# Kernel tuning notes

Measured on AMD Instinct MI355X. Metric: run time of the kernel, lower is better.

Reference implementation:

```python
import jax, jax.numpy as jnp
import numpy as np

N = 250000      # total nodes = B * NN
E = 4000000     # edges (avg degree 16)
NODE = 4        # node_size
EDGE = 1        # edge_size
HID = 32        # hidden_dim
NN = 50         # nnodes per graph
NF = 3          # num_factories


def setup_inputs() -> dict:
    key = jax.random.key(0)
    ks = jax.random.split(key, 10)
    def glorot(k, shp, fan_in):
        return (jax.random.normal(k, shp, jnp.float32) / np.sqrt(fan_in)).astype(jnp.float32)
    x = jax.random.normal(ks[0], (N, NODE), jnp.float32)
    edge_index = jax.random.randint(ks[1], (2, E), 0, N, dtype=jnp.int64)
    edge_attr = jax.random.normal(ks[2], (E, EDGE), jnp.float32)
    high = jnp.ones((NF,), jnp.float32)
    D_in = 2 * NODE + EDGE
    D_cat = NODE + HID
    W1 = glorot(ks[3], (D_in, HID), D_in); b1 = jnp.zeros((HID,), jnp.float32)
    W2 = glorot(ks[4], (HID, HID), HID);   b2 = jnp.zeros((HID,), jnp.float32)
    Wc = glorot(ks[5], (D_cat, 1), D_cat);  bc = jnp.zeros((1,), jnp.float32)
    Wmu = glorot(ks[6], (D_cat, 1), D_cat); bmu = jnp.zeros((1,), jnp.float32)
    Wsig = glorot(ks[7], (D_cat, 1), D_cat); bsig = jnp.zeros((1,), jnp.float32)
    return dict(x=x, edge_index=edge_index, edge_attr=edge_attr, high=high,
                W1=W1, b1=b1, W2=W2, b2=b2, Wc=Wc, bc=bc,
                Wmu=Wmu, bmu=bmu, Wsig=Wsig, bsig=bsig)


def reference(x, edge_index, edge_attr, high, W1, b1, W2, b2, Wc, bc, Wmu, bmu, Wsig, bsig):
    # EdgeConv (flow='target_to_source', aggr='add'): x_i = x[row], x_j = x[col], scatter-add at row
    row, col = edge_index[0], edge_index[1]
    msg_in = jnp.concatenate([x[row], x[col], edge_attr], axis=1)      # [E, 2*NODE+EDGE]
    msg = jax.nn.relu(msg_in @ W1 + b1) @ W2 + b2                      # [E, HID]
    agg = jax.ops.segment_sum(msg, row, num_segments=x.shape[0])       # [N, HID]
    x_pp = jnp.concatenate([x, agg], axis=1).reshape(-1, NN, NODE + HID)  # [B, NN, D_cat]
    tail = x_pp[:, -NF:]                                               # [B, NF, D_cat]
    alpha = jax.nn.softplus((tail @ Wmu + bmu).squeeze(-1) + 1e-20) + 1e-20   # [B, NF]
    beta = jax.nn.softplus((tail @ Wsig + bsig).squeeze(-1) + 1e-20) + 1e-20  # [B, NF]
    conc = jax.nn.softplus((x_pp @ Wc + bc).squeeze(-1) + 1e-10)       # [B, NN]
    inventory_act = conc / (conc.sum() + 1e-20)                        # deterministic Dirichlet mean-style
    order_act = alpha / (alpha + beta) * high                          # deterministic Beta mean * high
    return jnp.concatenate([inventory_act, order_act], axis=1)         # [B, NN+NF]
```

## Files before the change

kernel.cpp:

```cpp
#include <hip/hip_runtime.h>

#define N_NODES 250000
#define N_EDGES 4000000
#define HID 32
#define NN 50
#define NF 3
#define OUT_COLS (NN + NF)

#define NB 512
#define NBKT ((N_NODES + NB - 1) / NB)
#define PCHUNK 4096
#define NPBLK ((N_EDGES + PCHUNK - 1) / PCHUNK)
#define BCAP_SLOT 8832

typedef float float2v __attribute__((ext_vector_type(2)));

__device__ __forceinline__ float softplus_f(float v) {
    return fmaxf(v, 0.0f) + log1pf(expf(-fabsf(v)));
}

__device__ __forceinline__ float2v pk_fma(float a, float2v b, float2v c) {
    float2v av = {a, a};
    return __builtin_elementwise_fma(av, b, c);
}

__global__ __launch_bounds__(1024, 8) void part_kernel(
    const int* __restrict__ ei, const float* __restrict__ ea,
    int* __restrict__ gcursor, int2* __restrict__ bpay)
{
    __shared__ int2 srec[PCHUNK];
    __shared__ int  gdst[PCHUNK];
    __shared__ int hist[NBKT];
    __shared__ int excl[NBKT];
    __shared__ int gbase[NBKT];
    __shared__ int wsum[16];

    int t = threadIdx.x;
    int lane = t & 63, wid = t >> 6;
    int cbb = blockIdx.x * PCHUNK;
    int cnt = N_EDGES - cbb; if (cnt > PCHUNK) cnt = PCHUNK;

    for (int i = t; i < NBKT; i += 1024) hist[i] = 0;
    __syncthreads();

    int e0 = cbb + t * 4;
    int r[4], rk[4];
    bool full = (e0 + 4 <= N_EDGES);
    if (full) {
        int4 ra = *(const int4*)(ei + e0);
        r[0] = ra.x; r[1] = ra.y; r[2] = ra.z; r[3] = ra.w;
    } else {
        #pragma unroll
        for (int j = 0; j < 4; j++) r[j] = (e0 + j < N_EDGES) ? ei[e0 + j] : 0;
    }
    #pragma unroll
    for (int j = 0; j < 4; j++)
        rk[j] = (e0 + j < N_EDGES) ? atomicAdd(&hist[r[j] >> 9], 1) : 0;
    __syncthreads();

    int hv = (t < NBKT) ? hist[t] : 0;
    int v = hv;
    #pragma unroll
    for (int off = 1; off < 64; off <<= 1) {
        int u = __shfl_up(v, off, 64);
        if (lane >= off) v += u;
    }
    if (lane == 63) wsum[wid] = v;
    __syncthreads();
    if (wid == 0) {
        int w = (lane < 16) ? wsum[lane] : 0;
        #pragma unroll
        for (int off = 1; off < 16; off <<= 1) {
            int u = __shfl_up(w, off, 64);
            if (lane >= off) w += u;
        }
        if (lane < 16) wsum[lane] = w;
    }
    __syncthreads();
    int wbase = (wid > 0) ? wsum[wid - 1] : 0;
    int myExcl = wbase + (v - hv);
    if (t < NBKT) {
        excl[t] = myExcl;
        int base = 0;
        if (hv > 0) base = atomicAdd(&gcursor[t], hv);
        gbase[t] = t * BCAP_SLOT + base;
    }
    __syncthreads();

    if (full) {
        int4 ca = *(const int4*)(ei + N_EDGES + e0);
        float4 aa = *(const float4*)(ea + e0);
        int c[4] = {ca.x, ca.y, ca.z, ca.w};
        float a[4] = {aa.x, aa.y, aa.z, aa.w};
        #pragma unroll
        for (int j = 0; j < 4; j++) {
            int bb = r[j] >> 9;
            int lrow = r[j] & (NB - 1);
            int slot = excl[bb] + rk[j];
            int gpos = gbase[bb] + rk[j];
            srec[slot] = make_int2(c[j] | (lrow << 18), __float_as_int(a[j]));
            gdst[slot] = (gpos < (bb + 1) * BCAP_SLOT) ? gpos : -1;
        }
    } else {
        #pragma unroll
        for (int j = 0; j < 4; j++) {
            if (e0 + j < N_EDGES) {
                int bb = r[j] >> 9;
                int lrow = r[j] & (NB - 1);
                int col  = ei[N_EDGES + e0 + j];
                float at = ea[e0 + j];
                int slot = excl[bb] + rk[j];
                int gpos = gbase[bb] + rk[j];
                srec[slot] = make_int2(col | (lrow << 18), __float_as_int(at));
                gdst[slot] = (gpos < (bb + 1) * BCAP_SLOT) ? gpos : -1;
            }
        }
    }
    __syncthreads();

    for (int s = t; s < cnt; s += 1024) {
        int g = gdst[s];
        if (g >= 0) bpay[g] = srec[s];
    }
}

__global__ __launch_bounds__(512, 4) void bucket_kernel(
    const int2* __restrict__ bpay, const int* __restrict__ gcursor,
    const float* __restrict__ x,
    const float* __restrict__ W1, const float* __restrict__ b1,
    const float* __restrict__ W2, const float* __restrict__ b2,
    const float* __restrict__ Wc, const float* __restrict__ bc,
    const float* __restrict__ Wmu, const float* __restrict__ bmu,
    const float* __restrict__ Wsig, const float* __restrict__ bsig,
    const float* __restrict__ high,
    float* __restrict__ sum_out, float* __restrict__ out)
{
    __shared__ int2 srec[BCAP_SLOT];
    __shared__ int hist[NB];
    __shared__ int nbeg[NB];
    __shared__ int perm[NB];
    __shared__ int dhist[64];
    __shared__ int wsum[8];
    __shared__ float bsum[8];
    __shared__ float fW[3][32];
    __shared__ float fB[3];

    int b = blockIdx.x;
    int t = threadIdx.x;
    int lane = t & 63, wid = t >> 6;
    int beg = b * BCAP_SLOT;
    int cnt = gcursor[b]; if (cnt > BCAP_SLOT) cnt = BCAP_SLOT;

    hist[t] = 0;
    if (t < 96) {
        int vsel = t >> 5;
        int k = t & 31;
        const float* Wv = (vsel == 0) ? Wc : (vsel == 1) ? Wmu : Wsig;
        float f = 0.0f;
        #pragma unroll
        for (int j = 0; j < 32; j++) f = fmaf(W2[k * 32 + j], Wv[4 + j], f);
        fW[vsel][k] = f;
    } else if (t < 99) {
        int vsel = t - 96;
        const float* Wv = (vsel == 0) ? Wc : (vsel == 1) ? Wmu : Wsig;
        float f = 0.0f;
        #pragma unroll
        for (int j = 0; j < 32; j++) f = fmaf(b2[j], Wv[4 + j], f);
        fB[vsel] = f;
    }
    __syncthreads();

    int2 rec[18];
    int rk[18];
    #pragma unroll
    for (int k = 0; k < 9; k++) {
        int s = (k * 512 + t) * 2;
        int4 pp = *(const int4*)(bpay + beg + s);
        rec[2 * k]     = make_int2(pp.x, pp.y);
        rec[2 * k + 1] = make_int2(pp.z, pp.w);
        rk[2 * k]     = (s < cnt)     ? atomicAdd(&hist[(pp.x >> 18) & (NB - 1)], 1) : 0;
        rk[2 * k + 1] = (s + 1 < cnt) ? atomicAdd(&hist[(pp.z >> 18) & (NB - 1)], 1) : 0;
    }
    __syncthreads();

    int hv = hist[t];
    int v = hv;
    #pragma unroll
    for (int off = 1; off < 64; off <<= 1) {
        int u = __shfl_up(v, off, 64);
        if (lane >= off) v += u;
    }
    if (lane == 63) wsum[wid] = v;
    __syncthreads();
    if (wid == 0) {
        int w = (lane < 8) ? wsum[lane] : 0;
        #pragma unroll
        for (int off = 1; off < 8; off <<= 1) {
            int u = __shfl_up(w, off, 64);
            if (lane >= off) w += u;
        }
        if (lane < 8) wsum[lane] = w;
    }
    __syncthreads();
    int wbase = (wid > 0) ? wsum[wid - 1] : 0;
    nbeg[t] = wbase + (v - hv);
    __syncthreads();

    #pragma unroll
    for (int k = 0; k < 9; k++) {
        int s = (k * 512 + t) * 2;
        if (s < cnt) {
            int lrow = (rec[2 * k].x >> 18) & (NB - 1);
            srec[nbeg[lrow] + rk[2 * k]] = rec[2 * k];
        }
        if (s + 1 < cnt) {
            int lrow = (rec[2 * k + 1].x >> 18) & (NB - 1);
            srec[nbeg[lrow] + rk[2 * k + 1]] = rec[2 * k + 1];
        }
    }

    int bin = min(hv, 63);
    if (t < 64) dhist[t] = 0;
    __syncthreads();
    atomicAdd(&dhist[bin], 1);
    __syncthreads();
    if (wid == 0) {
        int dv = dhist[lane];
        int sv = dv;
        #pragma unroll
        for (int off = 1; off < 64; off <<= 1) {
            int u = __shfl_up(sv, off, 64);
            if (lane >= off) sv += u;
        }
        dhist[lane] = sv - dv;
    }
    __syncthreads();
    int pos = atomicAdd(&dhist[bin], 1);
    perm[pos] = t;
    __syncthreads();

    int tt = perm[t];
    int n = b * NB + tt;
    bool valid = (n < N_NODES);
    int nn = valid ? n : 0;
    int deg = valid ? hist[tt] : 0;
    int s0 = nbeg[tt];

    float4 xr = *(const float4*)(x + 4 * (size_t)nn);

    const float2v* W1v = (const float2v*)W1;
    const float2v* b1v = (const float2v*)b1;

    float2v arow[16];
    #pragma unroll
    for (int k2 = 0; k2 < 16; k2++) {
        float2v a = b1v[k2];
        a = pk_fma(xr.x, W1v[0 * 16 + k2], a);
        a = pk_fma(xr.y, W1v[1 * 16 + k2], a);
        a = pk_fma(xr.z, W1v[2 * 16 + k2], a);
        a = pk_fma(xr.w, W1v[3 * 16 + k2], a);
        arow[k2] = a;
    }

    float2v acc2[16];
    #pragma unroll
    for (int j2 = 0; j2 < 16; j2++) { float2v z = {0.f, 0.f}; acc2[j2] = z; }

    float mk0[4], ev0[4];
    float4 xc0[4];
    #pragma unroll
    for (int j = 0; j < 4; j++) {
        bool ok = j < deg;
        int idx = ok ? (s0 + j) : 0;
        int2 rr = srec[idx];
        mk0[j] = ok ? 1.0f : 0.0f;
        int col = ok ? (rr.x & 0x3FFFF) : 0;
        ev0[j] = ok ? __int_as_float(rr.y) : 0.0f;
        xc0[j] = *(const float4*)(x + 4 * (size_t)col);
    }

    for (int c = 0; c < deg; c += 4) {
        int c1 = c + 4;
        float mk1[4], ev1[4];
        float4 xc1[4];
        #pragma unroll
        for (int j = 0; j < 4; j++) {
            bool ok = (c1 + j) < deg;
            int idx = ok ? (s0 + c1 + j) : 0;
            int2 rr = srec[idx];
            mk1[j] = ok ? 1.0f : 0.0f;
            int col = ok ? (rr.x & 0x3FFFF) : 0;
            ev1[j] = ok ? __int_as_float(rr.y) : 0.0f;
            xc1[j] = *(const float4*)(x + 4 * (size_t)col);
        }

        #pragma unroll
        for (int k2 = 0; k2 < 16; k2++) {
            float2v w4 = W1v[4 * 16 + k2];
            float2v w5 = W1v[5 * 16 + k2];
            float2v w6 = W1v[6 * 16 + k2];
            float2v w7 = W1v[7 * 16 + k2];
            float2v w8 = W1v[8 * 16 + k2];
            #pragma unroll
            for (int j = 0; j < 4; j++) {
                float2v a = arow[k2];
                a = pk_fma(xc0[j].x, w4, a);
                a = pk_fma(xc0[j].y, w5, a);
                a = pk_fma(xc0[j].z, w6, a);
                a = pk_fma(xc0[j].w, w7, a);
                a = pk_fma(ev0[j],   w8, a);
                float2v zero = {0.0f, 0.0f};
                a = __builtin_elementwise_max(a, zero);
                float2v mm = {mk0[j], mk0[j]};
                acc2[k2] = __builtin_elementwise_fma(a, mm, acc2[k2]);
            }
        }

        #pragma unroll
        for (int j = 0; j < 4; j++) {
            mk0[j] = mk1[j]; ev0[j] = ev1[j]; xc0[j] = xc1[j];
        }
    }

    float c_val = 0.0f;
    if (valid) {
        float* accf = (float*)acc2;
        float fdeg = (float)deg;

        float zc = fmaf(fdeg, fB[0], bc[0]);
        zc = fmaf(xr.x, Wc[0], zc);
        zc = fmaf(xr.y, Wc[1], zc);
        zc = fmaf(xr.z, Wc[2], zc);
        zc = fmaf(xr.w, Wc[3], zc);
        #pragma unroll
        for (int j = 0; j < 32; j++) zc = fmaf(accf[j], fW[0][j], zc);
        c_val = softplus_f(zc + 1e-10f);

        int g = n / NN;
        int i = n - g * NN;
        out[(size_t)g * OUT_COLS + i] = c_val;

        if (i >= NN - NF) {
            float zm = fmaf(fdeg, fB[1], bmu[0]);
            float zs = fmaf(fdeg, fB[2], bsig[0]);
            zm = fmaf(xr.x, Wmu[0], zm);   zs = fmaf(xr.x, Wsig[0], zs);
            zm = fmaf(xr.y, Wmu[1], zm);   zs = fmaf(xr.y, Wsig[1], zs);
            zm = fmaf(xr.z, Wmu[2], zm);   zs = fmaf(xr.z, Wsig[2], zs);
            zm = fmaf(xr.w, Wmu[3], zm);   zs = fmaf(xr.w, Wsig[3], zs);
            #pragma unroll
            for (int j = 0; j < 32; j++) {
                zm = fmaf(accf[j], fW[1][j], zm);
                zs = fmaf(accf[j], fW[2][j], zs);
            }
            float alpha = softplus_f(zm + 1e-20f) + 1e-20f;
            float beta  = softplus_f(zs + 1e-20f) + 1e-20f;
            int k = i - (NN - NF);
            out[(size_t)g * OUT_COLS + NN + k] = alpha / (alpha + beta) * high[k];
        }
    }

    float s = c_val;
    #pragma unroll
    for (int off = 32; off > 0; off >>= 1) s += __shfl_down(s, off, 64);
    if (lane == 0) bsum[wid] = s;
    __syncthreads();
    if (t == 0) {
        float tt2 = 0.0f;
        #pragma unroll
        for (int j = 0; j < 8; j++) tt2 += bsum[j];
        atomicAdd(sum_out, tt2);
    }
}

__global__ __launch_bounds__(256) void div_kernel(
    const float* __restrict__ sum_in, float* __restrict__ out)
{
    int n = blockIdx.x * 256 + threadIdx.x;
    if (n >= N_NODES) return;
    float inv = 1.0f / (*sum_in + 1e-20f);
    int g = n / NN;
    int i = n - g * NN;
    out[(size_t)g * OUT_COLS + i] *= inv;
}

extern "C" void kernel_launch(void* const* d_in, const int* in_sizes, int n_in,
                              void* d_out, int out_size, void* d_ws, size_t ws_size,
                              hipStream_t stream)
{
    const float* x    = (const float*)d_in[0];
    const int*   ei   = (const int*)d_in[1];
    const float* ea   = (const float*)d_in[2];
    const float* high = (const float*)d_in[3];
    const float* W1   = (const float*)d_in[4];
    const float* b1   = (const float*)d_in[5];
    const float* W2   = (const float*)d_in[6];
    const float* b2   = (const float*)d_in[7];
    const float* Wc   = (const float*)d_in[8];
    const float* bc   = (const float*)d_in[9];
    const float* Wmu  = (const float*)d_in[10];
    const float* bmu  = (const float*)d_in[11];
    const float* Wsig = (const float*)d_in[12];
    const float* bsig = (const float*)d_in[13];
    float* out = (float*)d_out;

    char* ws = (char*)d_ws;
    int2*  bpay    = (int2*)ws;
    int*   gcursor = (int*)(ws + 34550784);
    float* ssum    = (float*)(ws + 34552832);

    hipMemsetAsync(gcursor, 0, 2052, stream);

    part_kernel<<<NPBLK, 1024, 0, stream>>>(ei, ea, gcursor, bpay);
    bucket_kernel<<<NBKT, 512, 0, stream>>>(
        bpay, gcursor, x, W1, b1, W2, b2, Wc, bc, Wmu, bmu, Wsig, bsig,
        high, ssum, out);
    div_kernel<<<(N_NODES + 255) / 256, 256, 0, stream>>>(ssum, out);
}
```

Baseline: 186.0 us.

## Halve node bucket size and split each node's edges across two threads

After: 201.2 us. +8.2%, slower.

```diff
diff --git a/kernel.cpp b/kernel.cpp
--- a/kernel.cpp
+++ b/kernel.cpp
@@ -7,11 +7,11 @@
 #define NF 3
 #define OUT_COLS (NN + NF)
 
-#define NB 512
+#define NB 256
 #define NBKT ((N_NODES + NB - 1) / NB)
 #define PCHUNK 4096
 #define NPBLK ((N_EDGES + PCHUNK - 1) / PCHUNK)
-#define BCAP_SLOT 8832
+#define BCAP_SLOT 4544
 
 typedef float float2v __attribute__((ext_vector_type(2)));
 
@@ -55,7 +55,7 @@
     }
     #pragma unroll
     for (int j = 0; j < 4; j++)
-        rk[j] = (e0 + j < N_EDGES) ? atomicAdd(&hist[r[j] >> 9], 1) : 0;
+        rk[j] = (e0 + j < N_EDGES) ? atomicAdd(&hist[r[j] >> 8], 1) : 0;
     __syncthreads();
 
     int hv = (t < NBKT) ? hist[t] : 0;
@@ -94,7 +94,7 @@
         float a[4] = {aa.x, aa.y, aa.z, aa.w};
         #pragma unroll
         for (int j = 0; j < 4; j++) {
-            int bb = r[j] >> 9;
+            int bb = r[j] >> 8;
             int lrow = r[j] & (NB - 1);
             int slot = excl[bb] + rk[j];
             int gpos = gbase[bb] + rk[j];
@@ -105,7 +105,7 @@
         #pragma unroll
         for (int j = 0; j < 4; j++) {
             if (e0 + j < N_EDGES) {
-                int bb = r[j] >> 9;
+                int bb = r[j] >> 8;
                 int lrow = r[j] & (NB - 1);
                 int col  = ei[N_EDGES + e0 + j];
                 float at = ea[e0 + j];
@@ -140,7 +140,7 @@
     __shared__ int nbeg[NB];
     __shared__ int perm[NB];
     __shared__ int dhist[64];
-    __shared__ int wsum[8];
+    __shared__ int wsum[4];
     __shared__ float bsum[8];
     __shared__ float fW[3][32];
     __shared__ float fB[3];
@@ -151,17 +151,17 @@
     int beg = b * BCAP_SLOT;
     int cnt = gcursor[b]; if (cnt > BCAP_SLOT) cnt = BCAP_SLOT;
 
-    hist[t] = 0;
-    if (t < 96) {
-        int vsel = t >> 5;
+    if (t < NB) hist[t] = 0;
+    if (t >= 256 && t < 352) {
+        int vsel = (t - 256) >> 5;
         int k = t & 31;
         const float* Wv = (vsel == 0) ? Wc : (vsel == 1) ? Wmu : Wsig;
         float f = 0.0f;
         #pragma unroll
         for (int j = 0; j < 32; j++) f = fmaf(W2[k * 32 + j], Wv[4 + j], f);
         fW[vsel][k] = f;
-    } else if (t < 99) {
-        int vsel = t - 96;
+    } else if (t >= 352 && t < 355) {
+        int vsel = t - 352;
         const float* Wv = (vsel == 0) ? Wc : (vsel == 1) ? Wmu : Wsig;
         float f = 0.0f;
         #pragma unroll
@@ -170,12 +170,13 @@
     }
     __syncthreads();
 
-    int2 rec[18];
-    int rk[18];
-    #pragma unroll
-    for (int k = 0; k < 9; k++) {
+    int2 rec[10];
+    int rk[10];
+    #pragma unroll
+    for (int k = 0; k < 5; k++) {
         int s = (k * 512 + t) * 2;
-        int4 pp = *(const int4*)(bpay + beg + s);
+        int sc = (s <= BCAP_SLOT - 2) ? s : 0;
+        int4 pp = *(const int4*)(bpay + beg + sc);
         rec[2 * k]     = make_int2(pp.x, pp.y);
         rec[2 * k + 1] = make_int2(pp.z, pp.w);
         rk[2 * k]     = (s < cnt)     ? atomicAdd(&hist[(pp.x >> 18) & (NB - 1)], 1) : 0;
@@ -183,31 +184,33 @@
     }
     __syncthreads();
 
-    int hv = hist[t];
+    int hv = (t < NB) ? hist[t] : 0;
     int v = hv;
     #pragma unroll
     for (int off = 1; off < 64; off <<= 1) {
         int u = __shfl_up(v, off, 64);
         if (lane >= off) v += u;
     }
-    if (lane == 63) wsum[wid] = v;
+    if (lane == 63 && wid < 4) wsum[wid] = v;
     __syncthreads();
     if (wid == 0) {
-        int w = (lane < 8) ? wsum[lane] : 0;
-        #pragma unroll
-        for (int off = 1; off < 8; off <<= 1) {
+        int w = (lane < 4) ? wsum[lane] : 0;
+        #pragma unroll
+        for (int off = 1; off < 4; off <<= 1) {
             int u = __shfl_up(w, off, 64);
             if (lane >= off) w += u;
         }
-        if (lane < 8) wsum[lane] = w;
-    }
-    __syncthreads();
-    int wbase = (wid > 0) ? wsum[wid - 1] : 0;
-    nbeg[t] = wbase + (v - hv);
-    __syncthreads();
-
-    #pragma unroll
-    for (int k = 0; k < 9; k++) {
+        if (lane < 4) wsum[lane] = w;
+    }
+    __syncthreads();
+    if (t < NB) {
+        int wbase = (wid > 0) ? wsum[wid - 1] : 0;
+        nbeg[t] = wbase + (v - hv);
+    }
+    __syncthreads();
+
+    #pragma unroll
+    for (int k = 0; k < 5; k++) {
         int s = (k * 512 + t) * 2;
         if (s < cnt) {
             int lrow = (rec[2 * k].x >> 18) & (NB - 1);
@@ -219,10 +222,10 @@
         }
     }
 
+    if (t < 64) dhist[t] = 0;
+    __syncthreads();
     int bin = min(hv, 63);
-    if (t < 64) dhist[t] = 0;
-    __syncthreads();
-    atomicAdd(&dhist[bin], 1);
+    if (t < NB) atomicAdd(&dhist[bin], 1);
     __syncthreads();
     if (wid == 0) {
         int dv = dhist[lane];
@@ -235,16 +238,22 @@
         dhist[lane] = sv - dv;
     }
     __syncthreads();
-    int pos = atomicAdd(&dhist[bin], 1);
-    perm[pos] = t;
-    __syncthreads();
-
-    int tt = perm[t];
-    int n = b * NB + tt;
+    if (t < NB) {
+        int pos = atomicAdd(&dhist[bin], 1);
+        perm[pos] = t;
+    }
+    __syncthreads();
+
+    int pr = t >> 1;
+    int slice = t & 1;
+    int node = perm[pr];
+    int n = b * NB + node;
     bool valid = (n < N_NODES);
     int nn = valid ? n : 0;
-    int deg = valid ? hist[tt] : 0;
-    int s0 = nbeg[tt];
+    int deg = valid ? hist[node] : 0;
+    int half = (deg + 1) >> 1;
+    int myCnt = slice ? (deg - half) : half;
+    int s0 = nbeg[node] + slice * half;
 
     float4 xr = *(const float4*)(x + 4 * (size_t)nn);
 
@@ -270,7 +279,7 @@
     float4 xc0[4];
     #pragma unroll
     for (int j = 0; j < 4; j++) {
-        bool ok = j < deg;
+        bool ok = j < myCnt;
         int idx = ok ? (s0 + j) : 0;
         int2 rr = srec[idx];
         mk0[j] = ok ? 1.0f : 0.0f;
@@ -279,13 +288,13 @@
         xc0[j] = *(const float4*)(x + 4 * (size_t)col);
     }
 
-    for (int c = 0; c < deg; c += 4) {
+    for (int c = 0; c < myCnt; c += 4) {
         int c1 = c + 4;
         float mk1[4], ev1[4];
         float4 xc1[4];
         #pragma unroll
         for (int j = 0; j < 4; j++) {
-            bool ok = (c1 + j) < deg;
+            bool ok = (c1 + j) < myCnt;
             int idx = ok ? (s0 + c1 + j) : 0;
             int2 rr = srec[idx];
             mk1[j] = ok ? 1.0f : 0.0f;
@@ -322,9 +331,12 @@
         }
     }
 
+    float* accf = (float*)acc2;
+    #pragma unroll
+    for (int j = 0; j < 32; j++) accf[j] += __shfl_xor(accf[j], 1, 64);
+
     float c_val = 0.0f;
-    if (valid) {
-        float* accf = (float*)acc2;
+    if (valid && slice == 0) {
         float fdeg = (float)deg;
 
         float zc = fmaf(fdeg, fB[0], bc[0]);
@@ -405,10 +417,10 @@
 
     char* ws = (char*)d_ws;
     int2*  bpay    = (int2*)ws;
-    int*   gcursor = (int*)(ws + 34550784);
-    float* ssum    = (float*)(ws + 34552832);
-
-    hipMemsetAsync(gcursor, 0, 2052, stream);
+    int*   gcursor = (int*)(ws + 35511296);
+    float* ssum    = (float*)(ws + 35515204);
+
+    hipMemsetAsync(gcursor, 0, 3912, stream);
 
     part_kernel<<<NPBLK, 1024, 0, stream>>>(ei, ea, gcursor, bpay);
     bucket_kernel<<<NBKT, 512, 0, stream>>>(
```
